# Optimization experiments

Hardware: AMD Instinct MI355X
Metric: run time of the kernel (lower is better)

The kernel has to match this reference:

```python
import jax, jax.numpy as jnp
import numpy as np

EPS = 0.05  # blend weight of K_Rectify smoothing


def k_rectify(x_nbc, distance, idx, eps=EPS):
    """Distance-weighted neighbor smoothing.
    x_nbc: (N, B, C); distance, idx: (B, N, K). Returns (N, B, C)."""
    x_bnc = jnp.transpose(x_nbc, (1, 0, 2))                       # (B,N,C)
    B = x_bnc.shape[0]
    neigh = x_bnc[jnp.arange(B)[:, None, None], idx]              # (B,N,K,C) gather
    w = jax.nn.softmax(-distance, axis=-1)                        # closer -> larger weight
    smoothed = jnp.einsum('bnk,bnkc->bnc', w, neigh)              # (B,N,C)
    y = (1.0 - eps) * x_bnc + eps * smoothed
    return jnp.transpose(y, (1, 0, 2))


def monarch_linear(x, w1, w2, bias):
    """Monarch block-diagonal butterfly multiply on the last dim.
    w1: (k,q,p), w2: (l,s,r) with k*p == n, l*r == k*q."""
    shp = x.shape
    k, q, p = w1.shape
    l, s, r = w2.shape
    xb = x.reshape(-1, k, p)
    o1 = jnp.einsum('kqp,bkp->bkq', w1, xb)                       # (B*, k, q)
    o1 = o1.reshape(-1, r, l).transpose(0, 2, 1)                  # 'b (r l) -> b l r'
    o2 = jnp.einsum('lsr,blr->bls', w2, o1)                       # (B*, l, s)
    out = o2.transpose(0, 2, 1).reshape(-1, s * l) + bias         # 'b l s -> b (s l)'
    return out.reshape(*shp[:-1], s * l)


def setup_inputs() -> dict:
    key = jax.random.key(0)
    B, N, C, K, nblocks = 8, 8192, 256, 8, 8
    blk = C // nblocks
    ks = jax.random.split(key, 6)
    x = jax.random.normal(ks[0], (B, N, C), dtype=jnp.float32)
    distance = jax.random.uniform(ks[1], (B, N, K), dtype=jnp.float32)
    idx = jax.random.randint(ks[2], (B, N, K), 0, N)
    rf = jax.random.normal(ks[3], (B, N, C), dtype=jnp.float32)
    scale = 1.0 / np.sqrt(blk)
    w1 = jax.random.normal(ks[4], (nblocks, blk, blk), dtype=jnp.float32) * scale
    w2 = jax.random.normal(ks[5], (nblocks, blk, blk), dtype=jnp.float32) * scale
    bias = jnp.zeros((C,), dtype=jnp.float32)
    return {"x": x, "distance": distance, "idx": idx, "rf": rf,
            "w1": w1, "w2": w2, "bias": bias}


def reference(x, distance, idx, rf, w1, w2, bias):
    # _prepare_in: (B,N,C) -> (N,B,C)
    xs = jnp.transpose(x, (1, 0, 2))
    s1 = k_rectify(xs, distance, idx)            # smooth_in
    t = monarch_linear(s1, w1, w2, bias)         # Monarch block-diag matmul
    s2 = k_rectify(t, distance, idx)             # smooth_out
    return jnp.transpose(s2, (1, 0, 2)) + rf     # _out_transform residual
```

## Files before the change

### kernel.cpp

```cpp
#include <hip/hip_runtime.h>

#define NPTS 8192
#define CH   256
#define KNB  8
#define NROWS 65536
#define ROWS_PER_BLK 32
#define ROWS_PER_IT  4
#define NIT (ROWS_PER_BLK / ROWS_PER_IT)
#define FT_STRIDE 36

#define NBLK_CONV 8192
#define NBLK_S1   (NROWS / ROWS_PER_BLK)
#define NBLK_S2   (NROWS / 16)

typedef unsigned short ushort_t;
typedef float  f32x4  __attribute__((ext_vector_type(4)));

#define BARRIER_LDS() do { \
    asm volatile("s_waitcnt lgkmcnt(0)" ::: "memory"); \
    __builtin_amdgcn_s_barrier(); \
} while (0)

__device__ __forceinline__ int xcd_swz(int h, int cpx) {
    return (h & 7) * cpx + (h >> 3);
}

__device__ __forceinline__ ushort_t f32_to_bf16(float f) {
    unsigned int b = __float_as_uint(f);
    b += 0x7FFFu + ((b >> 16) & 1u);
    return (ushort_t)(b >> 16);
}
__device__ __forceinline__ float bf16_to_f32(ushort_t u) {
    return __uint_as_float(((unsigned int)u) << 16);
}
__device__ __forceinline__ unsigned int pack_bf16(float lo, float hi) {
    return (unsigned int)f32_to_bf16(lo) | ((unsigned int)f32_to_bf16(hi) << 16);
}

__global__ __launch_bounds__(256) void pm_conv(
    const f32x4* __restrict__ x, uint4* __restrict__ xb)
{
    const int l = xcd_swz(blockIdx.x, NBLK_CONV / 8);
    const size_t i = (size_t)l * 256 + threadIdx.x;
    const f32x4 a = __builtin_nontemporal_load(&x[2 * i]);
    const f32x4 c = __builtin_nontemporal_load(&x[2 * i + 1]);
    uint4 o;
    o.x = pack_bf16(a.x, a.y);
    o.y = pack_bf16(a.z, a.w);
    o.z = pack_bf16(c.x, c.y);
    o.w = pack_bf16(c.z, c.w);
    xb[i] = o;
}

__global__ __launch_bounds__(256, 4) void pm_stage1(
    const ushort_t* __restrict__ xb, const float* __restrict__ dist,
    const int* __restrict__ idx, const float* __restrict__ w1,
    const float* __restrict__ w2, const float* __restrict__ bias,
    ushort_t* __restrict__ t)
{
    const int c = threadIdx.x;

    __shared__ float s1[ROWS_PER_IT][CH];
    __shared__ float fT[ROWS_PER_IT][8 * FT_STRIDE];

    float4 w1r[8], w2r[8];
    {
        const float4* w1p = (const float4*)(w1 + c * 32);
        const float4* w2p = (const float4*)(w2 + ((c & 7) * 32 + (c >> 3)) * 32);
#pragma unroll
        for (int i = 0; i < 8; ++i) { w1r[i] = w1p[i]; w2r[i] = w2p[i]; }
    }
    const float bb = bias[c];
    const int l2   = c & 7;
    const int kb   = c >> 5;
    const int ftw  = l2 * FT_STRIDE + (c >> 3);

    const int rr   = __builtin_amdgcn_readfirstlane(threadIdx.x >> 6);
    const int lane = threadIdx.x & 63;

    const int lb       = xcd_swz(blockIdx.x, NBLK_S1 / 8);
    const int row_base = lb * ROWS_PER_BLK;
    const int b = row_base >> 13;
    const char* xbase  = (const char*)(xb + (size_t)b * NPTS * CH);
    const int laneoff  = lane * 8;

    float dcur[KNB]; int nbs[KNB];
    {
        const int row = row_base + rr;
        const float4 d0 = *(const float4*)(dist + (size_t)row * KNB);
        const float4 d1 = *(const float4*)(dist + (size_t)row * KNB + 4);
        const int4   i0 = *(const int4*)(idx + (size_t)row * KNB);
        const int4   i1 = *(const int4*)(idx + (size_t)row * KNB + 4);
        dcur[0]=d0.x; dcur[1]=d0.y; dcur[2]=d0.z; dcur[3]=d0.w;
        dcur[4]=d1.x; dcur[5]=d1.y; dcur[6]=d1.z; dcur[7]=d1.w;
        nbs[0]=__builtin_amdgcn_readfirstlane(i0.x);
        nbs[1]=__builtin_amdgcn_readfirstlane(i0.y);
        nbs[2]=__builtin_amdgcn_readfirstlane(i0.z);
        nbs[3]=__builtin_amdgcn_readfirstlane(i0.w);
        nbs[4]=__builtin_amdgcn_readfirstlane(i1.x);
        nbs[5]=__builtin_amdgcn_readfirstlane(i1.y);
        nbs[6]=__builtin_amdgcn_readfirstlane(i1.z);
        nbs[7]=__builtin_amdgcn_readfirstlane(i1.w);
    }
    ushort4 c0, g[KNB];
    {
        const int rloc = (row_base + rr) & (NPTS - 1);
        c0 = *(const ushort4*)(xbase + ((size_t)rloc << 9) + laneoff);
#pragma unroll
        for (int k = 0; k < KNB; ++k)
            g[k] = *(const ushort4*)(xbase + ((size_t)(unsigned)nbs[k] << 9) + laneoff);
    }

    for (int it = 0; it < NIT; ++it) {
        const bool more = (it + 1 < NIT);
        const int rown  = row_base + (more ? it + 1 : it) * ROWS_PER_IT + rr;

        const float4 dn0 = *(const float4*)(dist + (size_t)rown * KNB);
        const float4 dn1 = *(const float4*)(dist + (size_t)rown * KNB + 4);
        const int4   in0 = *(const int4*)(idx + (size_t)rown * KNB);
        const int4   in1 = *(const int4*)(idx + (size_t)rown * KNB + 4);

        float mn = dcur[0];
#pragma unroll
        for (int k = 1; k < KNB; ++k) mn = fminf(mn, dcur[k]);
        float e[KNB]; float sum = 0.f;
#pragma unroll
        for (int k = 0; k < KNB; ++k) { e[k] = __expf(mn - dcur[k]); sum += e[k]; }
        const float inv = 0.05f / sum;

        float4 acc;
        acc.x = 0.95f * bf16_to_f32(c0.x);
        acc.y = 0.95f * bf16_to_f32(c0.y);
        acc.z = 0.95f * bf16_to_f32(c0.z);
        acc.w = 0.95f * bf16_to_f32(c0.w);
#pragma unroll
        for (int k = 0; k < KNB; ++k) {
            const float w = e[k] * inv;
            acc.x += w * bf16_to_f32(g[k].x);
            acc.y += w * bf16_to_f32(g[k].y);
            acc.z += w * bf16_to_f32(g[k].z);
            acc.w += w * bf16_to_f32(g[k].w);
        }
        ((float4*)&s1[rr][0])[lane] = acc;

        BARRIER_LDS();

#pragma unroll
        for (int r2 = 0; r2 < ROWS_PER_IT; ++r2) {
            const float4* sb = (const float4*)(&s1[r2][kb * 32]);
            float a = 0.f;
#pragma unroll
            for (int p4 = 0; p4 < 8; ++p4) {
                const float4 s = sb[p4];
                a += w1r[p4].x * s.x + w1r[p4].y * s.y
                   + w1r[p4].z * s.z + w1r[p4].w * s.w;
            }
            fT[r2][ftw] = a;
        }

        if (more) {
            dcur[0]=dn0.x; dcur[1]=dn0.y; dcur[2]=dn0.z; dcur[3]=dn0.w;
            dcur[4]=dn1.x; dcur[5]=dn1.y; dcur[6]=dn1.z; dcur[7]=dn1.w;
            nbs[0]=__builtin_amdgcn_readfirstlane(in0.x);
            nbs[1]=__builtin_amdgcn_readfirstlane(in0.y);
            nbs[2]=__builtin_amdgcn_readfirstlane(in0.z);
            nbs[3]=__builtin_amdgcn_readfirstlane(in0.w);
            nbs[4]=__builtin_amdgcn_readfirstlane(in1.x);
            nbs[5]=__builtin_amdgcn_readfirstlane(in1.y);
            nbs[6]=__builtin_amdgcn_readfirstlane(in1.z);
            nbs[7]=__builtin_amdgcn_readfirstlane(in1.w);
            const int rloc = rown & (NPTS - 1);
            c0 = *(const ushort4*)(xbase + ((size_t)rloc << 9) + laneoff);
#pragma unroll
            for (int k = 0; k < KNB; ++k)
                g[k] = *(const ushort4*)(xbase + ((size_t)(unsigned)nbs[k] << 9) + laneoff);
        }

        BARRIER_LDS();

#pragma unroll
        for (int r2 = 0; r2 < ROWS_PER_IT; ++r2) {
            const float4* fp = (const float4*)(&fT[r2][l2 * FT_STRIDE]);
            float a = bb;
#pragma unroll
            for (int r4 = 0; r4 < 8; ++r4) {
                const float4 f = fp[r4];
                a += w2r[r4].x * f.x + w2r[r4].y * f.y
                   + w2r[r4].z * f.z + w2r[r4].w * f.w;
            }
            t[(size_t)(row_base + it * ROWS_PER_IT + r2) * CH + c] = f32_to_bf16(a);
        }
    }
}

__global__ __launch_bounds__(256, 4) void pm_stage2(
    const ushort_t* __restrict__ t, const float* __restrict__ dist,
    const int* __restrict__ idx, const float* __restrict__ rf,
    float* __restrict__ out)
{
    const int w     = __builtin_amdgcn_readfirstlane(threadIdx.x >> 6);
    const int lane  = threadIdx.x & 63;
    const int lb    = xcd_swz(blockIdx.x, NBLK_S2 / 8);
    const int wrow0 = lb * 16 + w * 4;
    const int b     = wrow0 >> 13;
    const char* tbase = (const char*)(t + (size_t)b * NPTS * CH);
    const int laneoff = lane * 8;

    int   nbs[4][KNB];
    float d [4][KNB];
#pragma unroll
    for (int r = 0; r < 4; ++r) {
        const int row = wrow0 + r;
        const float4 d0 = *(const float4*)(dist + (size_t)row * KNB);
        const float4 d1 = *(const float4*)(dist + (size_t)row * KNB + 4);
        const int4   i0 = *(const int4*)(idx + (size_t)row * KNB);
        const int4   i1 = *(const int4*)(idx + (size_t)row * KNB + 4);
        d[r][0]=d0.x; d[r][1]=d0.y; d[r][2]=d0.z; d[r][3]=d0.w;
        d[r][4]=d1.x; d[r][5]=d1.y; d[r][6]=d1.z; d[r][7]=d1.w;
        nbs[r][0]=__builtin_amdgcn_readfirstlane(i0.x);
        nbs[r][1]=__builtin_amdgcn_readfirstlane(i0.y);
        nbs[r][2]=__builtin_amdgcn_readfirstlane(i0.z);
        nbs[r][3]=__builtin_amdgcn_readfirstlane(i0.w);
        nbs[r][4]=__builtin_amdgcn_readfirstlane(i1.x);
        nbs[r][5]=__builtin_amdgcn_readfirstlane(i1.y);
        nbs[r][6]=__builtin_amdgcn_readfirstlane(i1.z);
        nbs[r][7]=__builtin_amdgcn_readfirstlane(i1.w);
    }

    ushort4 c0[4], g[4][KNB];
    f32x4   rv[4];
#pragma unroll
    for (int r = 0; r < 4; ++r) {
        const int rloc = (wrow0 + r) & (NPTS - 1);
        c0[r] = *(const ushort4*)(tbase + ((size_t)rloc << 9) + laneoff);
        rv[r] = __builtin_nontemporal_load(
                    &((const f32x4*)rf)[(size_t)(wrow0 + r) * 64 + lane]);
#pragma unroll
        for (int k = 0; k < KNB; ++k)
            g[r][k] = *(const ushort4*)(tbase + ((size_t)(unsigned)nbs[r][k] << 9) + laneoff);
    }

#pragma unroll
    for (int r = 0; r < 4; ++r) {
        float mn = d[r][0];
#pragma unroll
        for (int k = 1; k < KNB; ++k) mn = fminf(mn, d[r][k]);
        float e[KNB]; float sum = 0.f;
#pragma unroll
        for (int k = 0; k < KNB; ++k) { e[k] = __expf(mn - d[r][k]); sum += e[k]; }
        const float inv = 0.05f / sum;

        f32x4 acc;
        acc.x = 0.95f * bf16_to_f32(c0[r].x) + rv[r].x;
        acc.y = 0.95f * bf16_to_f32(c0[r].y) + rv[r].y;
        acc.z = 0.95f * bf16_to_f32(c0[r].z) + rv[r].z;
        acc.w = 0.95f * bf16_to_f32(c0[r].w) + rv[r].w;
#pragma unroll
        for (int k = 0; k < KNB; ++k) {
            const float wk = e[k] * inv;
            acc.x += wk * bf16_to_f32(g[r][k].x);
            acc.y += wk * bf16_to_f32(g[r][k].y);
            acc.z += wk * bf16_to_f32(g[r][k].z);
            acc.w += wk * bf16_to_f32(g[r][k].w);
        }
        __builtin_nontemporal_store(
            acc, &((f32x4*)out)[(size_t)(wrow0 + r) * 64 + lane]);
    }
}

extern "C" void kernel_launch(void* const* d_in, const int* in_sizes, int n_in,
                              void* d_out, int out_size, void* d_ws, size_t ws_size,
                              hipStream_t stream) {
    const float* x    = (const float*)d_in[0];
    const float* dist = (const float*)d_in[1];
    const int*   idx  = (const int*)d_in[2];
    const float* rf   = (const float*)d_in[3];
    const float* w1   = (const float*)d_in[4];
    const float* w2   = (const float*)d_in[5];
    const float* bias = (const float*)d_in[6];
    float* out = (float*)d_out;

    ushort_t* t  = (ushort_t*)d_ws;
    ushort_t* xb = (ushort_t*)((char*)d_ws + (size_t)NROWS * CH * 2);

    pm_conv  <<<NBLK_CONV, 256, 0, stream>>>((const f32x4*)x, (uint4*)xb);
    pm_stage1<<<NBLK_S1,   256, 0, stream>>>(xb, dist, idx, w1, w2, bias, t);
    pm_stage2<<<NBLK_S2,   256, 0, stream>>>(t, dist, idx, rf, out);
}
```

Before: 265.3 us.

## Replace scalar Monarch matmuls in stage1 with bf16 MFMA over 32-row tiles

Stage1 now smooths all 32 rows of a block into a swizzled bf16 LDS tile, then computes both Monarch block-diagonal products with mfma_f32_16x16x32_bf16 instead of per-thread FMA dot products, and writes the output rows back coalesced through LDS. This removes the two barriers per 4-row iteration and the scalar FMA work. In exchange the intermediate after the first Monarch factor is rounded to bf16 (lower precision). Weights are also converted to bf16 from global memory on the fly in every block.

```diff
diff --git a/kernel.cpp b/kernel.cpp
--- a/kernel.cpp
+++ b/kernel.cpp
@@ -4,17 +4,14 @@
 #define CH   256
 #define KNB  8
 #define NROWS 65536
-#define ROWS_PER_BLK 32
-#define ROWS_PER_IT  4
-#define NIT (ROWS_PER_BLK / ROWS_PER_IT)
-#define FT_STRIDE 36
-
+#define RPB_S1 32
 #define NBLK_CONV 8192
-#define NBLK_S1   (NROWS / ROWS_PER_BLK)
+#define NBLK_S1   (NROWS / RPB_S1)
 #define NBLK_S2   (NROWS / 16)
 
 typedef unsigned short ushort_t;
 typedef float  f32x4  __attribute__((ext_vector_type(4)));
+typedef short  bf16x8 __attribute__((ext_vector_type(8)));
 
 #define BARRIER_LDS() do { \
     asm volatile("s_waitcnt lgkmcnt(0)" ::: "memory"); \
@@ -35,6 +32,12 @@
 }
 __device__ __forceinline__ unsigned int pack_bf16(float lo, float hi) {
     return (unsigned int)f32_to_bf16(lo) | ((unsigned int)f32_to_bf16(hi) << 16);
+}
+__device__ __forceinline__ bf16x8 pack8w(const float* __restrict__ p) {
+    bf16x8 r;
+#pragma unroll
+    for (int j = 0; j < 8; ++j) r[j] = (short)f32_to_bf16(p[j]);
+    return r;
 }
 
 __global__ __launch_bounds__(256) void pm_conv(
@@ -58,35 +61,21 @@
     const float* __restrict__ w2, const float* __restrict__ bias,
     ushort_t* __restrict__ t)
 {
-    const int c = threadIdx.x;
-
-    __shared__ float s1[ROWS_PER_IT][CH];
-    __shared__ float fT[ROWS_PER_IT][8 * FT_STRIDE];
-
-    float4 w1r[8], w2r[8];
-    {
-        const float4* w1p = (const float4*)(w1 + c * 32);
-        const float4* w2p = (const float4*)(w2 + ((c & 7) * 32 + (c >> 3)) * 32);
-#pragma unroll
-        for (int i = 0; i < 8; ++i) { w1r[i] = w1p[i]; w2r[i] = w2p[i]; }
-    }
-    const float bb = bias[c];
-    const int l2   = c & 7;
-    const int kb   = c >> 5;
-    const int ftw  = l2 * FT_STRIDE + (c >> 3);
-
-    const int rr   = __builtin_amdgcn_readfirstlane(threadIdx.x >> 6);
     const int lane = threadIdx.x & 63;
+    const int wv   = __builtin_amdgcn_readfirstlane(threadIdx.x >> 6);
+
+    __shared__ __align__(16) unsigned char s1b[RPB_S1 * 512];
+    __shared__ __align__(16) unsigned char fsb[RPB_S1 * 512];
 
     const int lb       = xcd_swz(blockIdx.x, NBLK_S1 / 8);
-    const int row_base = lb * ROWS_PER_BLK;
-    const int b = row_base >> 13;
+    const int row_base = lb * RPB_S1;
+    const int b        = row_base >> 13;
     const char* xbase  = (const char*)(xb + (size_t)b * NPTS * CH);
     const int laneoff  = lane * 8;
 
     float dcur[KNB]; int nbs[KNB];
     {
-        const int row = row_base + rr;
+        const int row = row_base + wv;
         const float4 d0 = *(const float4*)(dist + (size_t)row * KNB);
         const float4 d1 = *(const float4*)(dist + (size_t)row * KNB + 4);
         const int4   i0 = *(const int4*)(idx + (size_t)row * KNB);
@@ -104,21 +93,16 @@
     }
     ushort4 c0, g[KNB];
     {
-        const int rloc = (row_base + rr) & (NPTS - 1);
+        const int rloc = (row_base + wv) & (NPTS - 1);
         c0 = *(const ushort4*)(xbase + ((size_t)rloc << 9) + laneoff);
 #pragma unroll
         for (int k = 0; k < KNB; ++k)
             g[k] = *(const ushort4*)(xbase + ((size_t)(unsigned)nbs[k] << 9) + laneoff);
     }
 
-    for (int it = 0; it < NIT; ++it) {
-        const bool more = (it + 1 < NIT);
-        const int rown  = row_base + (more ? it + 1 : it) * ROWS_PER_IT + rr;
-
-        const float4 dn0 = *(const float4*)(dist + (size_t)rown * KNB);
-        const float4 dn1 = *(const float4*)(dist + (size_t)rown * KNB + 4);
-        const int4   in0 = *(const int4*)(idx + (size_t)rown * KNB);
-        const int4   in1 = *(const int4*)(idx + (size_t)rown * KNB + 4);
+#pragma unroll
+    for (int p = 0; p < 8; ++p) {
+        const int rl = p * 4 + wv;
 
         float mn = dcur[0];
 #pragma unroll
@@ -127,6 +111,15 @@
 #pragma unroll
         for (int k = 0; k < KNB; ++k) { e[k] = __expf(mn - dcur[k]); sum += e[k]; }
         const float inv = 0.05f / sum;
+
+        float4 dn0, dn1; int4 in0, in1;
+        if (p < 7) {
+            const int rown = row_base + (p + 1) * 4 + wv;
+            dn0 = *(const float4*)(dist + (size_t)rown * KNB);
+            dn1 = *(const float4*)(dist + (size_t)rown * KNB + 4);
+            in0 = *(const int4*)(idx + (size_t)rown * KNB);
+            in1 = *(const int4*)(idx + (size_t)rown * KNB + 4);
+        }
 
         float4 acc;
         acc.x = 0.95f * bf16_to_f32(c0.x);
@@ -141,24 +134,12 @@
             acc.z += w * bf16_to_f32(g[k].z);
             acc.w += w * bf16_to_f32(g[k].w);
         }
-        ((float4*)&s1[rr][0])[lane] = acc;
-
-        BARRIER_LDS();
-
-#pragma unroll
-        for (int r2 = 0; r2 < ROWS_PER_IT; ++r2) {
-            const float4* sb = (const float4*)(&s1[r2][kb * 32]);
-            float a = 0.f;
-#pragma unroll
-            for (int p4 = 0; p4 < 8; ++p4) {
-                const float4 s = sb[p4];
-                a += w1r[p4].x * s.x + w1r[p4].y * s.y
-                   + w1r[p4].z * s.z + w1r[p4].w * s.w;
-            }
-            fT[r2][ftw] = a;
-        }
-
-        if (more) {
+        uint2 pv;
+        pv.x = pack_bf16(acc.x, acc.y);
+        pv.y = pack_bf16(acc.z, acc.w);
+        *(uint2*)(s1b + rl * 512 + ((lane * 8) ^ ((rl & 7) << 4))) = pv;
+
+        if (p < 7) {
             dcur[0]=dn0.x; dcur[1]=dn0.y; dcur[2]=dn0.z; dcur[3]=dn0.w;
             dcur[4]=dn1.x; dcur[5]=dn1.y; dcur[6]=dn1.z; dcur[7]=dn1.w;
             nbs[0]=__builtin_amdgcn_readfirstlane(in0.x);
@@ -169,27 +150,89 @@
             nbs[5]=__builtin_amdgcn_readfirstlane(in1.y);
             nbs[6]=__builtin_amdgcn_readfirstlane(in1.z);
             nbs[7]=__builtin_amdgcn_readfirstlane(in1.w);
-            const int rloc = rown & (NPTS - 1);
+            const int rloc = (row_base + (p + 1) * 4 + wv) & (NPTS - 1);
             c0 = *(const ushort4*)(xbase + ((size_t)rloc << 9) + laneoff);
 #pragma unroll
             for (int k = 0; k < KNB; ++k)
                 g[k] = *(const ushort4*)(xbase + ((size_t)(unsigned)nbs[k] << 9) + laneoff);
         }
-
-        BARRIER_LDS();
-
-#pragma unroll
-        for (int r2 = 0; r2 < ROWS_PER_IT; ++r2) {
-            const float4* fp = (const float4*)(&fT[r2][l2 * FT_STRIDE]);
-            float a = bb;
-#pragma unroll
-            for (int r4 = 0; r4 < 8; ++r4) {
-                const float4 f = fp[r4];
-                a += w2r[r4].x * f.x + w2r[r4].y * f.y
-                   + w2r[r4].z * f.z + w2r[r4].w * f.w;
+    }
+
+    BARRIER_LDS();
+
+    const int l15 = lane & 15;
+    const int kq  = lane >> 4;
+#pragma unroll
+    for (int kk = 0; kk < 2; ++kk) {
+        const int kb = wv * 2 + kk;
+        const int ao = (kb * 64 + kq * 16);
+        const bf16x8 a0 = *(const bf16x8*)(s1b + l15 * 512        + (ao ^ ((l15 & 7) << 4)));
+        const bf16x8 a1 = *(const bf16x8*)(s1b + (16 + l15) * 512 + (ao ^ (((16 + l15) & 7) << 4)));
+        const bf16x8 b0 = pack8w(w1 + (size_t)(kb * 32 + l15) * 32 + kq * 8);
+        const bf16x8 b1 = pack8w(w1 + (size_t)(kb * 32 + 16 + l15) * 32 + kq * 8);
+        f32x4 d00 = {0.f,0.f,0.f,0.f}, d01 = d00, d10 = d00, d11 = d00;
+        d00 = __builtin_amdgcn_mfma_f32_16x16x32_bf16(a0, b0, d00, 0, 0, 0);
+        d01 = __builtin_amdgcn_mfma_f32_16x16x32_bf16(a0, b1, d01, 0, 0, 0);
+        d10 = __builtin_amdgcn_mfma_f32_16x16x32_bf16(a1, b0, d10, 0, 0, 0);
+        d11 = __builtin_amdgcn_mfma_f32_16x16x32_bf16(a1, b1, d11, 0, 0, 0);
+#pragma unroll
+        for (int nt = 0; nt < 2; ++nt) {
+            const int qq = nt * 16 + l15;
+            const int fo = (qq & 7) * 64 + (kb * 4 + (qq >> 3)) * 2;
+#pragma unroll
+            for (int mt = 0; mt < 2; ++mt) {
+                const f32x4 dd = (mt == 0) ? (nt == 0 ? d00 : d01)
+                                           : (nt == 0 ? d10 : d11);
+#pragma unroll
+                for (int reg = 0; reg < 4; ++reg) {
+                    const int row = mt * 16 + kq * 4 + reg;
+                    *(ushort_t*)(fsb + row * 512 + (fo ^ ((row & 7) << 4))) =
+                        f32_to_bf16(dd[reg]);
+                }
             }
-            t[(size_t)(row_base + it * ROWS_PER_IT + r2) * CH + c] = f32_to_bf16(a);
-        }
+        }
+    }
+
+    BARRIER_LDS();
+
+#pragma unroll
+    for (int kk = 0; kk < 2; ++kk) {
+        const int l2 = wv * 2 + kk;
+        const int ao = (l2 * 64 + kq * 16);
+        const bf16x8 a0 = *(const bf16x8*)(fsb + l15 * 512        + (ao ^ ((l15 & 7) << 4)));
+        const bf16x8 a1 = *(const bf16x8*)(fsb + (16 + l15) * 512 + (ao ^ (((16 + l15) & 7) << 4)));
+        const bf16x8 b0 = pack8w(w2 + (size_t)(l2 * 32 + l15) * 32 + kq * 8);
+        const bf16x8 b1 = pack8w(w2 + (size_t)(l2 * 32 + 16 + l15) * 32 + kq * 8);
+        f32x4 d00 = {0.f,0.f,0.f,0.f}, d01 = d00, d10 = d00, d11 = d00;
+        d00 = __builtin_amdgcn_mfma_f32_16x16x32_bf16(a0, b0, d00, 0, 0, 0);
+        d01 = __builtin_amdgcn_mfma_f32_16x16x32_bf16(a0, b1, d01, 0, 0, 0);
+        d10 = __builtin_amdgcn_mfma_f32_16x16x32_bf16(a1, b0, d10, 0, 0, 0);
+        d11 = __builtin_amdgcn_mfma_f32_16x16x32_bf16(a1, b1, d11, 0, 0, 0);
+#pragma unroll
+        for (int nt = 0; nt < 2; ++nt) {
+            const int cD = (nt * 16 + l15) * 8 + l2;
+            const float bv = bias[cD];
+#pragma unroll
+            for (int mt = 0; mt < 2; ++mt) {
+                const f32x4 dd = (mt == 0) ? (nt == 0 ? d00 : d01)
+                                           : (nt == 0 ? d10 : d11);
+#pragma unroll
+                for (int reg = 0; reg < 4; ++reg) {
+                    const int row = mt * 16 + kq * 4 + reg;
+                    *(ushort_t*)(s1b + row * 512 + cD * 2) =
+                        f32_to_bf16(dd[reg] + bv);
+                }
+            }
+        }
+    }
+
+    BARRIER_LDS();
+
+#pragma unroll
+    for (int r = 0; r < 8; ++r) {
+        const int row = wv * 8 + r;
+        const uint2 v = *(const uint2*)(s1b + row * 512 + lane * 8);
+        *(uint2*)((char*)t + ((size_t)(row_base + row) << 9) + lane * 8) = v;
     }
 }
 
```

Result: faster. 238.6 us (-10.1%).
